# Optimization experiments

Measured on AMD Instinct MI355X. Metric: run time of the kernel, lower is better.

The kernel has to match this reference:

```python
import jax, jax.numpy as jnp
import numpy as np

B, D, K = 8192, 1024, 128
LR = 0.5        # model_args.kmeans_lr, momentum coefficient
EPS = 1e-8      # torch CosineSimilarity eps
NEG_MASK = -10000.0


def setup_inputs() -> dict:
    key = jax.random.key(0)
    k1, k2, k3 = jax.random.split(key, 3)
    return {
        "datapoints": jax.random.normal(k1, (B, D), dtype=jnp.float32),
        "centroid": jax.random.normal(k2, (K, D), dtype=jnp.float32),
        "batch_cos_sim": jax.random.uniform(k3, (B, B), dtype=jnp.float32),
    }


def _cosine_rows(x, y):
    # cosine similarity between every row of x [N,d] and every row of y [M,d]
    xn = x / jnp.maximum(jnp.linalg.norm(x, axis=-1, keepdims=True), EPS)
    yn = y / jnp.maximum(jnp.linalg.norm(y, axis=-1, keepdims=True), EPS)
    return xn @ yn.T  # [N, M]


def reference(datapoints, centroid, batch_cos_sim):
    k = centroid.shape[0]
    b = datapoints.shape[0]

    # cosine sim to centroids (temp = 1)
    intra_cos_sim = _cosine_rows(datapoints, centroid)          # [B, K]

    # hard assignment
    dp_index = jnp.argmax(intra_cos_sim, axis=-1)               # [B]
    onehot = jax.nn.one_hot(dp_index, k, dtype=datapoints.dtype)  # [B, K]

    # intra-class adjacency: same-cluster indicator minus self-loops
    dp_cluster = onehot @ onehot.T - jnp.eye(b, dtype=datapoints.dtype)  # [B, B]

    # gather assigned centroid per datapoint
    dp_centroid = centroid[dp_index]                            # [B, D]

    # hard negative: second-closest centroid
    _, top2_idx = jax.lax.top_k(intra_cos_sim, 2)
    hard_negative = centroid[top2_idx[:, 1]]                    # [B, D]

    # false-negative mask: same-cluster pairs more similar than own centroid
    dp_centroid_cos = jnp.max(intra_cos_sim, axis=-1, keepdims=True)     # [B, 1]
    inter_class_mask = dp_cluster * (batch_cos_sim > dp_centroid_cos)
    cos_mask = inter_class_mask * NEG_MASK                      # [B, B]

    # momentum k-means centroid update
    cluster_sum = onehot.T @ datapoints                         # [K, D]
    updated = (jnp.sum(onehot, axis=0) > 0)[:, None]            # [K, 1] bool
    data = cluster_sum + centroid * (~updated).astype(centroid.dtype)
    new_centroid = LR * data + (1.0 - LR) * centroid            # [K, D]

    return dp_centroid, dp_cluster, hard_negative, cos_mask, new_centroid
```

## Files before the change

### kernel.cpp

```cpp
#include <hip/hip_runtime.h>
#include <cmath>

#define B_N 8192
#define D_N 1024
#define K_N 128

typedef float float4v __attribute__((ext_vector_type(4)));


__device__ __forceinline__ void row_norm2(const float* __restrict__ src, int row,
                                          double* __restrict__ out) {
  int lane = threadIdx.x & 63;
  const float4* s4 = (const float4*)(src + (size_t)row * D_N);
  double acc = 0.0;
#pragma unroll
  for (int e = 0; e < 4; ++e) {
    float4 v = s4[e * 64 + lane];
    acc += (double)v.x * v.x + (double)v.y * v.y + (double)v.z * v.z + (double)v.w * v.w;
  }
#pragma unroll
  for (int off = 32; off; off >>= 1) acc += __shfl_xor(acc, off, 64);
  if (lane == 0) out[row] = acc;
}

__global__ __launch_bounds__(256) void prep_k(const float* __restrict__ dp,
                                              const float* __restrict__ cent,
                                              float* __restrict__ ct,
                                              double* __restrict__ xnorm2,
                                              double* __restrict__ cnorm2) {
  int bid = blockIdx.x;
  if (bid < 512) {
    int e = bid * 256 + threadIdx.x;
    int k = e >> 10, d = e & 1023;
    ct[d * K_N + k] = cent[e];
  } else if (bid < 2560) {
    int w = threadIdx.x >> 6;
    row_norm2(dp, (bid - 512) * 4 + w, xnorm2);
  } else {
    int w = threadIdx.x >> 6;
    row_norm2(cent, (bid - 2560) * 4 + w, cnorm2);
  }
}

__global__ __launch_bounds__(256, 3) void assign_part_k(const float* __restrict__ dp,
                                                        const float* __restrict__ ct,
                                                        float* __restrict__ pdot) {
  __shared__ __align__(16) float xs[64 * 64];
  __shared__ __align__(16) float cs[64 * K_N];
  const int tid = threadIdx.x;
  const int rg = tid >> 5;
  const int cg = tid & 31;
  const int h = blockIdx.x >> 7;
  const int rowbase = (blockIdx.x & 127) * 64;
  const int dbase = h * 256;

  float a32[8][4];
  double a64[8][4];
#pragma unroll
  for (int r = 0; r < 8; ++r)
#pragma unroll
    for (int q = 0; q < 4; ++q) a64[r][q] = 0.0;

  for (int ch = 0; ch < 4; ++ch) {
    const int db = dbase + ch * 64;
#pragma unroll
    for (int i = 0; i < 4; ++i) {
      int fid = tid + i * 256;
      int r = fid >> 4, c4 = (fid & 15) * 4;
      *(float4*)&xs[r * 64 + c4] =
          *(const float4*)&dp[(size_t)(rowbase + r) * D_N + db + c4];
    }
#pragma unroll
    for (int i = 0; i < 8; ++i) {
      int fid = tid + i * 256;
      int dd = fid >> 5, kq = (fid & 31) * 4;
      *(float4*)&cs[dd * K_N + kq] =
          *(const float4*)&ct[(size_t)(db + dd) * K_N + kq];
    }
    __syncthreads();

#pragma unroll
    for (int r = 0; r < 8; ++r)
#pragma unroll
      for (int q = 0; q < 4; ++q) a32[r][q] = 0.0f;

    for (int dd = 0; dd < 64; dd += 4) {
      float4 cf[4];
#pragma unroll
      for (int e = 0; e < 4; ++e)
        cf[e] = *(const float4*)&cs[(dd + e) * K_N + cg * 4];
#pragma unroll
      for (int r = 0; r < 8; ++r) {
        float4 xv = *(const float4*)&xs[(rg * 8 + r) * 64 + dd];
        a32[r][0] += xv.x * cf[0].x + xv.y * cf[1].x + xv.z * cf[2].x + xv.w * cf[3].x;
        a32[r][1] += xv.x * cf[0].y + xv.y * cf[1].y + xv.z * cf[2].y + xv.w * cf[3].y;
        a32[r][2] += xv.x * cf[0].z + xv.y * cf[1].z + xv.z * cf[2].z + xv.w * cf[3].z;
        a32[r][3] += xv.x * cf[0].w + xv.y * cf[1].w + xv.z * cf[2].w + xv.w * cf[3].w;
      }
    }
#pragma unroll
    for (int r = 0; r < 8; ++r)
#pragma unroll
      for (int q = 0; q < 4; ++q) a64[r][q] += (double)a32[r][q];
    __syncthreads();
  }

  float* base = pdot + (size_t)h * B_N * K_N;
#pragma unroll
  for (int r = 0; r < 8; ++r) {
    int row = rowbase + rg * 8 + r;
    float4 v = make_float4((float)a64[r][0], (float)a64[r][1],
                           (float)a64[r][2], (float)a64[r][3]);
    *(float4*)(base + (size_t)row * K_N + cg * 4) = v;
  }
}

__global__ __launch_bounds__(256) void top2_gather_k(const float* __restrict__ pdot,
                                                     const double* __restrict__ xnorm2,
                                                     const double* __restrict__ cnorm2,
                                                     const float* __restrict__ cent,
                                                     int* __restrict__ dpidx,
                                                     double* __restrict__ maxcos,
                                                     float* __restrict__ out0,
                                                     float* __restrict__ out2) {
  const int w = threadIdx.x >> 6, l = threadIdx.x & 63;
  const int row = blockIdx.x * 4 + w;
  double s0 = 0.0, s1 = 0.0;
#pragma unroll
  for (int h = 0; h < 4; ++h) {
    float2 p = *(const float2*)&pdot[(size_t)h * B_N * K_N + (size_t)row * K_N + 2 * l];
    s0 += (double)p.x; s1 += (double)p.y;
  }
  double xinv = 1.0 / fmax(sqrt(xnorm2[row]), 1e-8);
  double2 cn = *(const double2*)&cnorm2[2 * l];
  double c0 = s0 * xinv / fmax(sqrt(cn.x), 1e-8);
  double c1 = s1 * xinv / fmax(sqrt(cn.y), 1e-8);

  double v1, v2; int i1, i2;
  if (c0 >= c1) { v1 = c0; i1 = 2 * l;     v2 = c1; i2 = 2 * l + 1; }
  else          { v1 = c1; i1 = 2 * l + 1; v2 = c0; i2 = 2 * l; }

#pragma unroll
  for (int off = 1; off < 64; off <<= 1) {
    double pv1 = __shfl_xor(v1, off, 64), pv2 = __shfl_xor(v2, off, 64);
    int    pi1 = __shfl_xor(i1, off, 64), pi2 = __shfl_xor(i2, off, 64);
    bool pb = (pv1 > v1) || (pv1 == v1 && pi1 < i1);
    double w1v = pb ? pv1 : v1;  int w1i = pb ? pi1 : i1;
    double lv  = pb ? v1  : pv1; int li  = pb ? i1  : pi1;
    double sv  = pb ? pv2 : v2;  int si  = pb ? pi2 : i2;
    bool lb = (lv > sv) || (lv == sv && li < si);
    v1 = w1v; i1 = w1i;
    v2 = lb ? lv : sv; i2 = lb ? li : si;
  }
  if (l == 0) { dpidx[row] = i1; maxcos[row] = v1; }

  const float4* g1 = (const float4*)(cent + (size_t)i1 * D_N);
  const float4* g2 = (const float4*)(cent + (size_t)i2 * D_N);
  float4* o0 = (float4*)(out0 + (size_t)row * D_N);
  float4* o2 = (float4*)(out2 + (size_t)row * D_N);
#pragma unroll
  for (int e = 0; e < 4; ++e) {
    o0[e * 64 + l] = g1[e * 64 + l];
    o2[e * 64 + l] = g2[e * 64 + l];
  }
}

__global__ __launch_bounds__(256) void maskpart_k(const float* __restrict__ batch,
                                                  const float* __restrict__ dp,
                                                  const int* __restrict__ dpidx,
                                                  const double* __restrict__ maxcos,
                                                  float* __restrict__ out1,
                                                  float* __restrict__ out3,
                                                  double* __restrict__ psum,
                                                  int* __restrict__ pcnt,
                                                  int nch, int npart) {
  __shared__ __align__(16) int cid[B_N];
  const int bid = blockIdx.x;
  const int t = threadIdx.x;
  if (bid < npart) {
    const int k = bid & 127;
    const int ch = bid >> 7;
    const int rows = B_N / nch;
    const int r0 = ch * rows;
    double a0 = 0, a1 = 0, a2 = 0, a3 = 0;
    int cnt = 0;
    for (int r = r0; r < r0 + rows; r += 4) {
      int4 q = *(const int4*)&dpidx[r];
      if (q.x == k) { float4 v = *(const float4*)&dp[(size_t)(r + 0) * D_N + t * 4];
                      a0 += v.x; a1 += v.y; a2 += v.z; a3 += v.w; ++cnt; }
      if (q.y == k) { float4 v = *(const float4*)&dp[(size_t)(r + 1) * D_N + t * 4];
                      a0 += v.x; a1 += v.y; a2 += v.z; a3 += v.w; ++cnt; }
      if (q.z == k) { float4 v = *(const float4*)&dp[(size_t)(r + 2) * D_N + t * 4];
                      a0 += v.x; a1 += v.y; a2 += v.z; a3 += v.w; ++cnt; }
      if (q.w == k) { float4 v = *(const float4*)&dp[(size_t)(r + 3) * D_N + t * 4];
                      a0 += v.x; a1 += v.y; a2 += v.z; a3 += v.w; ++cnt; }
    }
    double* o = psum + ((size_t)(ch * 128 + k)) * D_N + t * 4;
    o[0] = a0; o[1] = a1; o[2] = a2; o[3] = a3;
    if (t == 0) pcnt[ch * 128 + k] = cnt;
  } else {
#pragma unroll
    for (int i = 0; i < 8; ++i) {
      int idx = (t + i * 256) * 4;
      *(int4*)&cid[idx] = *(const int4*)&dpidx[idx];
    }
    __syncthreads();
    const int rb0 = (bid - npart) * 4;
    for (int rr = 0; rr < 4; ++rr) {
      const int i = rb0 + rr;
      const int ci = cid[i];
      const double thr = maxcos[i];
      const size_t rb = (size_t)i * B_N;
#pragma unroll 2
      for (int it = 0; it < 8; ++it) {
        int j = it * 1024 + t * 4;
        int4 c4 = *(const int4*)&cid[j];
        int m0 = (c4.x == ci) & ((j + 0) != i);
        int m1 = (c4.y == ci) & ((j + 1) != i);
        int m2 = (c4.z == ci) & ((j + 2) != i);
        int m3 = (c4.w == ci) & ((j + 3) != i);
        float4v bv = (float4v){0.f, 0.f, 0.f, 0.f};
        if (m0 | m1 | m2 | m3)
          bv = __builtin_nontemporal_load((const float4v*)&batch[rb + j]);
        float4v cl = (float4v){(float)m0, (float)m1, (float)m2, (float)m3};
        float4v mk = (float4v){
            (m0 && ((double)bv.x > thr)) ? -10000.f : 0.f,
            (m1 && ((double)bv.y > thr)) ? -10000.f : 0.f,
            (m2 && ((double)bv.z > thr)) ? -10000.f : 0.f,
            (m3 && ((double)bv.w > thr)) ? -10000.f : 0.f};
        __builtin_nontemporal_store(cl, (float4v*)&out1[rb + j]);
        __builtin_nontemporal_store(mk, (float4v*)&out3[rb + j]);
      }
    }
  }
}

__global__ __launch_bounds__(256) void finalize_k(const float* __restrict__ cent,
                                                  const double* __restrict__ psum,
                                                  const int* __restrict__ pcnt,
                                                  float* __restrict__ out4,
                                                  int nch) {
  int e = blockIdx.x * 256 + threadIdx.x;
  int k = e >> 10;
  int cnt = 0;
  double s = 0.0;
  for (int ch = 0; ch < nch; ++ch) {
    cnt += pcnt[ch * 128 + k];
    s += psum[(size_t)(ch * 128 + k) * D_N + (e & 1023)];
  }
  float c = cent[e];
  out4[e] = (cnt > 0) ? (float)(0.5 * s + 0.5 * (double)c) : c;
}

extern "C" void kernel_launch(void* const* d_in, const int* in_sizes, int n_in,
                              void* d_out, int out_size, void* d_ws, size_t ws_size,
                              hipStream_t stream) {
  const float* dp    = (const float*)d_in[0];
  const float* cent  = (const float*)d_in[1];
  const float* batch = (const float*)d_in[2];

  float* out  = (float*)d_out;
  float* out0 = out;
  float* out1 = out0 + 8388608;
  float* out2 = out1 + 67108864;
  float* out3 = out2 + 8388608;
  float* out4 = out3 + 67108864;

  char* w = (char*)d_ws;
  double* xnorm2 = (double*)(w + 0);
  double* cnorm2 = (double*)(w + 65536);
  int*    dpidx  = (int*)(w + 66560);
  double* maxcos = (double*)(w + 99328);
  float*  ct     = (float*)(w + 164864);
  float*  pdot   = (float*)(w + 689152);
  const size_t psum_base = 689152 + 16777216;

  int nch = 16;
  while (nch > 1 &&
         psum_base + (size_t)nch * (128ull * 1024 * 8 + 128 * 4) > ws_size)
    nch >>= 1;
  double* psum = (double*)(w + psum_base);
  int*    pcnt = (int*)(w + psum_base + (size_t)nch * 128 * 1024 * 8);
  const int npart = 128 * nch;

  prep_k<<<dim3(2592), dim3(256), 0, stream>>>(dp, cent, ct, xnorm2, cnorm2);
  assign_part_k<<<dim3(512), dim3(256), 0, stream>>>(dp, ct, pdot);
  top2_gather_k<<<dim3(2048), dim3(256), 0, stream>>>(pdot, xnorm2, cnorm2, cent,
                                                      dpidx, maxcos, out0, out2);
  maskpart_k<<<dim3(npart + 2048), dim3(256), 0, stream>>>(batch, dp, dpidx, maxcos,
                                                           out1, out3, psum, pcnt,
                                                           nch, npart);
  finalize_k<<<dim3(512), dim3(256), 0, stream>>>(cent, psum, pcnt, out4, nch);
}
```

Measured before the change: 248.1 us.

## Replace LDS-tiled assignment GEMM with register-direct global loads

The centroid-dot kernel stops staging datapoint and centroid tiles in shared memory and drops both barriers per chunk. Each thread now loads its operands straight from global memory (expected to hit L1/L2) and computes a 4x4 tile instead of 8x4. The grid doubles to 1024 blocks to raise parallelism. The cost is more global and cache traffic, since each thread re-fetches centroid columns and datapoint rows, and less reuse per thread.

```diff
diff --git a/kernel.cpp b/kernel.cpp
--- a/kernel.cpp
+++ b/kernel.cpp
@@ -42,76 +42,58 @@
   }
 }
 
-__global__ __launch_bounds__(256, 3) void assign_part_k(const float* __restrict__ dp,
-                                                        const float* __restrict__ ct,
-                                                        float* __restrict__ pdot) {
-  __shared__ __align__(16) float xs[64 * 64];
-  __shared__ __align__(16) float cs[64 * K_N];
+__global__ __launch_bounds__(256) void assign_reg_k(const float* __restrict__ dp,
+                                                    const float* __restrict__ ct,
+                                                    float* __restrict__ pdot) {
+  const int h = blockIdx.x >> 8;
+  const int rowbase = (blockIdx.x & 255) * 32;
+  const int dbase = h * 256;
   const int tid = threadIdx.x;
-  const int rg = tid >> 5;
-  const int cg = tid & 31;
-  const int h = blockIdx.x >> 7;
-  const int rowbase = (blockIdx.x & 127) * 64;
-  const int dbase = h * 256;
-
-  float a32[8][4];
-  double a64[8][4];
-#pragma unroll
-  for (int r = 0; r < 8; ++r)
+  const int rg = tid >> 5, cg2 = tid & 31;
+  double a64[4][4];
+#pragma unroll
+  for (int r = 0; r < 4; ++r)
 #pragma unroll
     for (int q = 0; q < 4; ++q) a64[r][q] = 0.0;
 
   for (int ch = 0; ch < 4; ++ch) {
     const int db = dbase + ch * 64;
-#pragma unroll
-    for (int i = 0; i < 4; ++i) {
-      int fid = tid + i * 256;
-      int r = fid >> 4, c4 = (fid & 15) * 4;
-      *(float4*)&xs[r * 64 + c4] =
-          *(const float4*)&dp[(size_t)(rowbase + r) * D_N + db + c4];
-    }
-#pragma unroll
-    for (int i = 0; i < 8; ++i) {
-      int fid = tid + i * 256;
-      int dd = fid >> 5, kq = (fid & 31) * 4;
-      *(float4*)&cs[dd * K_N + kq] =
-          *(const float4*)&ct[(size_t)(db + dd) * K_N + kq];
-    }
-    __syncthreads();
-
-#pragma unroll
-    for (int r = 0; r < 8; ++r)
+    float a32[4][4];
+#pragma unroll
+    for (int r = 0; r < 4; ++r)
 #pragma unroll
       for (int q = 0; q < 4; ++q) a32[r][q] = 0.0f;
 
+#pragma unroll 2
     for (int dd = 0; dd < 64; dd += 4) {
-      float4 cf[4];
+      float4 cf[4], xv[4];
 #pragma unroll
       for (int e = 0; e < 4; ++e)
-        cf[e] = *(const float4*)&cs[(dd + e) * K_N + cg * 4];
-#pragma unroll
-      for (int r = 0; r < 8; ++r) {
-        float4 xv = *(const float4*)&xs[(rg * 8 + r) * 64 + dd];
-        a32[r][0] += xv.x * cf[0].x + xv.y * cf[1].x + xv.z * cf[2].x + xv.w * cf[3].x;
-        a32[r][1] += xv.x * cf[0].y + xv.y * cf[1].y + xv.z * cf[2].y + xv.w * cf[3].y;
-        a32[r][2] += xv.x * cf[0].z + xv.y * cf[1].z + xv.z * cf[2].z + xv.w * cf[3].z;
-        a32[r][3] += xv.x * cf[0].w + xv.y * cf[1].w + xv.z * cf[2].w + xv.w * cf[3].w;
+        cf[e] = *(const float4*)&ct[(size_t)(db + dd + e) * K_N + cg2 * 4];
+#pragma unroll
+      for (int r = 0; r < 4; ++r)
+        xv[r] = *(const float4*)&dp[(size_t)(rowbase + rg * 4 + r) * D_N + db + dd];
+#pragma unroll
+      for (int r = 0; r < 4; ++r) {
+        a32[r][0] += xv[r].x * cf[0].x + xv[r].y * cf[1].x + xv[r].z * cf[2].x + xv[r].w * cf[3].x;
+        a32[r][1] += xv[r].x * cf[0].y + xv[r].y * cf[1].y + xv[r].z * cf[2].y + xv[r].w * cf[3].y;
+        a32[r][2] += xv[r].x * cf[0].z + xv[r].y * cf[1].z + xv[r].z * cf[2].z + xv[r].w * cf[3].z;
+        a32[r][3] += xv[r].x * cf[0].w + xv[r].y * cf[1].w + xv[r].z * cf[2].w + xv[r].w * cf[3].w;
       }
     }
 #pragma unroll
-    for (int r = 0; r < 8; ++r)
+    for (int r = 0; r < 4; ++r)
 #pragma unroll
       for (int q = 0; q < 4; ++q) a64[r][q] += (double)a32[r][q];
-    __syncthreads();
   }
 
   float* base = pdot + (size_t)h * B_N * K_N;
 #pragma unroll
-  for (int r = 0; r < 8; ++r) {
-    int row = rowbase + rg * 8 + r;
+  for (int r = 0; r < 4; ++r) {
+    int row = rowbase + rg * 4 + r;
     float4 v = make_float4((float)a64[r][0], (float)a64[r][1],
                            (float)a64[r][2], (float)a64[r][3]);
-    *(float4*)(base + (size_t)row * K_N + cg * 4) = v;
+    *(float4*)(base + (size_t)row * K_N + cg2 * 4) = v;
   }
 }
 
@@ -284,7 +266,7 @@
   const int npart = 128 * nch;
 
   prep_k<<<dim3(2592), dim3(256), 0, stream>>>(dp, cent, ct, xnorm2, cnorm2);
-  assign_part_k<<<dim3(512), dim3(256), 0, stream>>>(dp, ct, pdot);
+  assign_reg_k<<<dim3(1024), dim3(256), 0, stream>>>(dp, ct, pdot);
   top2_gather_k<<<dim3(2048), dim3(256), 0, stream>>>(pdot, xnorm2, cnorm2, cent,
                                                       dpidx, maxcos, out0, out2);
   maskpart_k<<<dim3(npart + 2048), dim3(256), 0, stream>>>(batch, dp, dpidx, maxcos,
```

Measured after the change: 269.9 us. +8.8%, slower.
